# Optimization experiments

Measured on AMD Instinct MI355X. Metric: run time of the kernel, lower is better.

## Reference

```python
import jax, jax.numpy as jnp
import numpy as np

L = 2        # n_layers
F = 128      # in_features == out_features (GRUCell + highway constraint)
O = 128
N = 1024     # nodes
B = 8        # batch
D = 3        # edge directions (weight.size(0))


def setup_inputs() -> dict:
    key = jax.random.key(0)
    ks = jax.random.split(key, 10)
    s = 1.0 / np.sqrt(F)
    u = lambda k, shp: jax.random.uniform(k, shp, jnp.float32, minval=-s, maxval=s)
    return {
        "inputs": jax.random.normal(ks[0], (N, B, F), jnp.float32),
        "adj": jax.random.uniform(ks[1], (D, B, N, N), jnp.float32),
        "W": u(ks[2], (L, D, F, O)),            # GCN weight per layer/direction
        "Bc": u(ks[3], (L, D, O)),              # GCN bias
        "Wh": u(ks[4], (L, F, O)),              # highway weight
        "Bh": u(ks[5], (L, O)),                 # highway bias
        "Wih": u(ks[6], (L, 3 * O, O)),         # GRUCell input weights
        "Whh": u(ks[7], (L, 3 * O, O)),         # GRUCell hidden weights
        "bih": u(ks[8], (L, 3 * O)),
        "bhh": u(ks[9], (L, 3 * O)),
    }


def _gru(x, h, wih, whh, bih, bhh):
    # torch.nn.GRUCell semantics; x,h: [..., O]
    gi = x @ wih.T + bih
    gh = h @ whh.T + bhh
    i_r, i_z, i_n = jnp.split(gi, 3, axis=-1)
    h_r, h_z, h_n = jnp.split(gh, 3, axis=-1)
    r = jax.nn.sigmoid(i_r + h_r)
    z = jax.nn.sigmoid(i_z + h_z)
    n = jnp.tanh(i_n + r * h_n)
    return (1.0 - z) * n + z * h


def reference(inputs, adj, W, Bc, Wh, Bh, Wih, Whh, bih, bhh):
    x = inputs  # [N, B, F]; dropout layers are identity at eval
    for l in range(L):
        # support per direction: [D, B, N, O]
        support = jnp.einsum('nbf,dfo->dbno', x, W[l]) + Bc[l][:, None, None, :]
        # adjacency-weighted aggregation: adj[d,b] @ support[d,b]
        agg = jnp.einsum('dbmn,dbno->dbmo', adj, support)
        # GRU update with hidden = current features, per direction, summed over d
        h = jnp.broadcast_to(jnp.transpose(x, (1, 0, 2))[None], agg.shape)
        hnew = _gru(agg, h, Wih[l], Whh[l], bih[l], bhh[l])
        out = jnp.transpose(jnp.sum(hnew, axis=0), (1, 0, 2))  # [N, B, O]
        out = jax.nn.relu(out)  # activation='relu'
        # highway gate (highway='relu')
        t = jax.nn.relu(jnp.einsum('nbf,fo->nbo', x, Wh[l]) + Bh[l])
        x = out * t + x * (1.0 - t)
    return x
```

## Files before the change

kernel.cpp:

```cpp
#include <hip/hip_runtime.h>
#include <math.h>

#define N_NODES 1024
#define BATCH   8
#define FEAT    128
#define NDIR    3
#define NB      (N_NODES*BATCH)
#define G3      384

typedef __bf16 bf16_t;
using bf16x8 = __attribute__((ext_vector_type(8))) __bf16;
using bf16x4 = __attribute__((ext_vector_type(4))) __bf16;
using f32x4  = __attribute__((ext_vector_type(4))) float;

#define GLOAD_LDS16(g, l) \
    __builtin_amdgcn_global_load_lds((const __attribute__((address_space(1))) void*)(g), \
                                     (__attribute__((address_space(3))) void*)(l), 16, 0, 0)

template<int R>
__device__ __forceinline__ void stage_swz(const bf16_t* __restrict__ src, int stride,
                                          int k0, bf16_t* lds, int w, int lane)
{
    #pragma unroll
    for (int q = 0; q < R/32; ++q) {
        int rbase = w*(R/4) + q*8;
        int row = rbase + (lane >> 3);
        int seg = (lane & 7) ^ (row & 7);
        GLOAD_LDS16(src + (size_t)row*stride + k0 + seg*8,
                    (char*)lds + (size_t)rbase*128);
    }
}

__device__ __forceinline__ void stageA_f32(const float* __restrict__ src, int k0,
                                           bf16_t* lds, int w, int lane)
{
    #pragma unroll
    for (int q = 0; q < 2; ++q) {
        int rbase = w*16 + q*8;
        int row = rbase + (lane >> 3);
        int s   = lane & 7;
        int seg = s ^ (row & 7);
        const float* g = src + (size_t)row*1024 + k0 + seg*8;
        float4 v0 = *reinterpret_cast<const float4*>(g);
        float4 v1 = *reinterpret_cast<const float4*>(g + 4);
        bf16x8 pk;
        pk[0]=(bf16_t)(v0.x-0.5f); pk[1]=(bf16_t)(v0.y-0.5f);
        pk[2]=(bf16_t)(v0.z-0.5f); pk[3]=(bf16_t)(v0.w-0.5f);
        pk[4]=(bf16_t)(v1.x-0.5f); pk[5]=(bf16_t)(v1.y-0.5f);
        pk[6]=(bf16_t)(v1.z-0.5f); pk[7]=(bf16_t)(v1.w-0.5f);
        *reinterpret_cast<bf16x8*>(&lds[row*64 + s*8]) = pk;
    }
}

template<int MI, int NJ>
__device__ __forceinline__ void mfma_swz(const bf16_t* As, const bf16_t* Bs,
                                         f32x4 (&acc)[MI][NJ], int wr, int wc, int lane)
{
    #pragma unroll
    for (int ks = 0; ks < 64; ks += 32) {
        int bslot = ks/8 + (lane >> 4);
        int sx = bslot ^ (lane & 7);
        bf16x8 af[MI], bfv[NJ];
        #pragma unroll
        for (int i = 0; i < MI; ++i) {
            int row = wr*MI*16 + i*16 + (lane & 15);
            af[i] = *reinterpret_cast<const bf16x8*>(&As[row*64 + sx*8]);
        }
        #pragma unroll
        for (int j = 0; j < NJ; ++j) {
            int row = wc*NJ*16 + j*16 + (lane & 15);
            bfv[j] = *reinterpret_cast<const bf16x8*>(&Bs[row*64 + sx*8]);
        }
        #pragma unroll
        for (int i = 0; i < MI; ++i) {
            #pragma unroll
            for (int j = 0; j < NJ; ++j)
                acc[i][j] = __builtin_amdgcn_mfma_f32_16x16x32_bf16(af[i], bfv[j], acc[i][j], 0, 0, 0);
        }
    }
}

__device__ __forceinline__ float fast_sigmoid(float x)
{
    float t = __builtin_amdgcn_exp2f(-1.442695041f * x);
    return __builtin_amdgcn_rcpf(1.0f + t);
}
__device__ __forceinline__ float fast_tanh(float x)
{
    float ax = fabsf(x);
    float t = __builtin_amdgcn_exp2f(-2.885390082f * ax);
    float r = (1.0f - t) * __builtin_amdgcn_rcpf(1.0f + t);
    return copysignf(r, x);
}

__global__ __launch_bounds__(128) void k_wprep(
    const float* __restrict__ W, const float* __restrict__ Wh,
    const float* __restrict__ Whh, const float* __restrict__ Wih,
    bf16_t* __restrict__ wsup,
    bf16_t* __restrict__ wihc)
{
    int m = blockIdx.x, l = blockIdx.y, k = threadIdx.x;
    float w;
    bf16_t* dst;
    bool patB = false;
    if (m < 384) {
        int d = m >> 7, o = m & 127;
        w = W[((size_t)(l*3 + d)*128 + k)*128 + o];
        dst = wsup + ((size_t)l*896 + m)*384;
    } else if (m < 512) {
        int o = m - 384;
        w = Wh[((size_t)l*128 + k)*128 + o];
        dst = wsup + ((size_t)l*896 + m)*384;
    } else if (m < 896) {
        int c = m - 512;
        w = Whh[((size_t)l*384 + c)*128 + k];
        dst = wsup + ((size_t)l*896 + m)*384;
    } else {
        int c = m - 896;
        w = Wih[((size_t)l*384 + c)*128 + k];
        dst = wihc + ((size_t)l*384 + c)*384;
        patB = true;
    }
    bf16_t hi = (bf16_t)w;
    bf16_t lo = (bf16_t)(w - (float)hi);
    if (patB) { dst[k] = hi; dst[128 + k] = hi; dst[256 + k] = lo; }
    else      { dst[k] = hi; dst[128 + k] = lo; dst[256 + k] = hi; }
}

__global__ __launch_bounds__(256) void k_xcat(
    const float* __restrict__ X, bf16_t* __restrict__ xcat,
    float* __restrict__ colsum2)
{
    int idx = blockIdx.x * 256 + threadIdx.x;
    if (idx < 2*3072) colsum2[idx] = 0.0f;
    int k = idx & 127, r = idx >> 7;
    int n = r >> 3, b = r & 7;
    float v = X[idx];
    bf16_t hi = (bf16_t)v;
    bf16_t lo = (bf16_t)(v - (float)hi);
    bf16_t* dst = xcat + ((size_t)(b*1024 + n))*384 + k;
    dst[0] = hi; dst[128] = hi; dst[256] = lo;
}

__global__ __launch_bounds__(256, 2) void k_sup2(
    const bf16_t* __restrict__ Wcat,
    const bf16_t* __restrict__ xcat,
    const float* __restrict__ Bcl,
    const float* __restrict__ Bhl,
    const float* __restrict__ bhhl,
    bf16_t* __restrict__ supt,
    float* __restrict__ tbuf,
    bf16_t* __restrict__ ghb,
    float* __restrict__ colsum)
{
    __shared__ bf16_t As[2][128*64];
    __shared__ bf16_t Bs[2][128*64];
    const int t = threadIdx.x, lane = t & 63, w = t >> 6;
    const int wr = w >> 1, wc = w & 1;
    const int n0 = blockIdx.x * 128;
    const int m0 = blockIdx.y * 128;
    const int b  = blockIdx.z;
    const bf16_t* Arow = Wcat + (size_t)m0 * 384;
    const bf16_t* Brow = xcat + ((size_t)b * 1024 + n0) * 384;

    f32x4 acc[4][4] = {};
    stage_swz<128>(Arow, 384, 0, As[0], w, lane);
    stage_swz<128>(Brow, 384, 0, Bs[0], w, lane);
    __syncthreads();
    #pragma unroll
    for (int kt = 0; kt < 6; ++kt) {
        if (kt + 1 < 6) {
            stage_swz<128>(Arow, 384, (kt+1)*64, As[(kt+1)&1], w, lane);
            stage_swz<128>(Brow, 384, (kt+1)*64, Bs[(kt+1)&1], w, lane);
        }
        mfma_swz<4,4>(As[kt&1], Bs[kt&1], acc, wr, wc, lane);
        __syncthreads();
    }
    #pragma unroll
    for (int i = 0; i < 4; ++i) {
        int mb = m0 + wr*64 + i*16 + ((lane >> 4) * 4);
        if (mb < 384) {
            #pragma unroll
            for (int rg = 0; rg < 4; ++rg) {
                int m = mb + rg;
                int d = m >> 7, o = m & 127;
                float bv = Bcl[d*128 + o];
                float psum = 0.0f;
                #pragma unroll
                for (int j = 0; j < 4; ++j) {
                    int n = n0 + wc*64 + j*16 + (lane & 15);
                    bf16_t sv = (bf16_t)(acc[i][j][rg] + bv);
                    supt[((size_t)((d*8 + b)*128 + o))*1024 + n] = sv;
                    psum += (float)sv;
                }
                psum += __shfl_xor(psum, 1, 64);
                psum += __shfl_xor(psum, 2, 64);
                psum += __shfl_xor(psum, 4, 64);
                psum += __shfl_xor(psum, 8, 64);
                if ((lane & 15) == 0)
                    atomicAdd(&colsum[(d*8 + b)*128 + o], psum);
            }
        } else if (mb < 512) {
            #pragma unroll
            for (int j = 0; j < 4; ++j) {
                int n = n0 + wc*64 + j*16 + (lane & 15);
                #pragma unroll
                for (int rg = 0; rg < 4; ++rg) {
                    int o = mb + rg - 384;
                    tbuf[((size_t)(b*128 + o))*1024 + n] =
                        fmaxf(acc[i][j][rg] + Bhl[o], 0.0f);
                }
            }
        } else {
            #pragma unroll
            for (int j = 0; j < 4; ++j) {
                int n = n0 + wc*64 + j*16 + (lane & 15);
                int c = mb - 512;
                bf16x4 pk;
                #pragma unroll
                for (int rg = 0; rg < 4; ++rg)
                    pk[rg] = (bf16_t)(acc[i][j][rg] + bhhl[c + rg]);
                *reinterpret_cast<bf16x4*>(&ghb[((size_t)(b*1024 + n))*384 + c]) = pk;
            }
        }
    }
}

__device__ __forceinline__ int aggls_off(int row, int k)
{
    return row*256 + (((k >> 3) ^ (row & 15)) << 3) + (k & 7);
}

__global__ __launch_bounds__(256, 2) void k_aggi(
    const float* __restrict__ adjf,
    const bf16_t* __restrict__ supt,
    const float* __restrict__ colsum,
    const bf16_t* __restrict__ wihcL,
    const float* __restrict__ biasL,
    bf16_t* __restrict__ girz,
    float* __restrict__ gin)
{
    __shared__ char pool[49152];
    __shared__ bf16_t aggls[64*256];
    bf16_t* As  = (bf16_t*)pool;
    bf16_t* Bs  = (bf16_t*)(pool + 16384);
    bf16_t* BsG = (bf16_t*)pool;

    const int t = threadIdx.x, lane = t & 63, w = t >> 6;
    const int wr = w >> 1, wc = w & 1;
    const int m0 = blockIdx.x * 64;
    const int z  = blockIdx.y;
    const float*  Af   = adjf + (size_t)z * 1024 * 1024 + (size_t)m0 * 1024;
    const bf16_t* Brow = supt + (size_t)z * 128 * 1024;

    f32x4 acc[2][4] = {};
    stageA_f32(Af, 0, As, w, lane);
    stage_swz<128>(Brow, 1024, 0, Bs, w, lane);
    __syncthreads();
    #pragma unroll
    for (int kt = 0; kt < 16; ++kt) {
        if (kt + 1 < 16) {
            stageA_f32(Af, (kt+1)*64, As + ((kt+1)&1)*4096, w, lane);
            stage_swz<128>(Brow, 1024, (kt+1)*64, Bs + ((kt+1)&1)*8192, w, lane);
        }
        mfma_swz<2,4>(As + (kt&1)*4096, Bs + (kt&1)*8192, acc, wr, wc, lane);
        __syncthreads();
    }

    stage_swz<128>(wihcL, 384, 0, BsG, w, lane);

    #pragma unroll
    for (int i = 0; i < 2; ++i) {
        #pragma unroll
        for (int rg = 0; rg < 4; ++rg) {
            int row = wr*32 + i*16 + ((lane >> 4) * 4) + rg;
            #pragma unroll
            for (int j = 0; j < 4; ++j) {
                int o = wc*64 + j*16 + (lane & 15);
                float v = acc[i][j][rg] + 0.5f * colsum[z*128 + o];
                bf16_t hi = (bf16_t)v;
                bf16_t lo = (bf16_t)(v - (float)hi);
                aggls[aggls_off(row, o)]       = hi;
                aggls[aggls_off(row, 128 + o)] = lo;
            }
        }
    }
    __syncthreads();

    #pragma unroll
    for (int cc = 0; cc < 3; ++cc) {
        f32x4 a2[2][4] = {};
        #pragma unroll
        for (int kt = 0; kt < 6; ++kt) {
            int it = cc*6 + kt;
            if (it + 1 < 18) {
                int nc = (it+1)/6, nk = (it+1)%6;
                stage_swz<128>(wihcL + (size_t)nc*128*384, 384, nk*64,
                               BsG + ((it+1)&1)*8192, w, lane);
            }
            const bf16_t* Bcur = BsG + (it&1)*8192;
            int akk = (kt < 4 ? kt : kt - 4) * 64;
            #pragma unroll
            for (int ks = 0; ks < 64; ks += 32) {
                bf16x8 af[2], bfv[4];
                #pragma unroll
                for (int i = 0; i < 2; ++i) {
                    int row = wr*32 + i*16 + (lane & 15);
                    int ss = ((akk + ks)/8 + (lane >> 4)) ^ (lane & 15);
                    af[i] = *reinterpret_cast<const bf16x8*>(&aggls[row*256 + ss*8]);
                }
                #pragma unroll
                for (int j = 0; j < 4; ++j) {
                    int row = wc*64 + j*16 + (lane & 15);
                    int sx = (ks/8 + (lane >> 4)) ^ (lane & 7);
                    bfv[j] = *reinterpret_cast<const bf16x8*>(&Bcur[row*64 + sx*8]);
                }
                #pragma unroll
                for (int i = 0; i < 2; ++i) {
                    #pragma unroll
                    for (int j = 0; j < 4; ++j)
                        a2[i][j] = __builtin_amdgcn_mfma_f32_16x16x32_bf16(af[i], bfv[j], a2[i][j], 0, 0, 0);
                }
            }
            __syncthreads();
        }
        #pragma unroll
        for (int j = 0; j < 4; ++j) {
            int c = cc*128 + wc*64 + j*16 + (lane & 15);
            float bv = biasL[c];
            #pragma unroll
            for (int i = 0; i < 2; ++i) {
                #pragma unroll
                for (int rg = 0; rg < 4; ++rg) {
                    int rloc = wr*32 + i*16 + ((lane >> 4) * 4) + rg;
                    size_t m = (size_t)z*1024 + m0 + rloc;
                    float v = a2[i][j][rg] + bv;
                    if (c < 256) girz[m*256 + c] = (bf16_t)v;
                    else         gin[m*128 + (c - 256)] = v;
                }
            }
        }
    }
}

__global__ __launch_bounds__(256) void k_gates(
    const bf16_t* __restrict__ girz, const float* __restrict__ gin,
    const bf16_t* __restrict__ ghb,
    bf16_t* xcat,
    const float* __restrict__ tbuf,
    float* __restrict__ Xout, int write_xcat)
{
    __shared__ float ts[128*17];
    const int b = blockIdx.y, n0 = blockIdx.x * 16;
    const int tid = threadIdx.x;
    {
        int o = tid >> 1, nh = (tid & 1) * 8;
        const float* src = tbuf + ((size_t)(b*128 + o))*1024 + n0 + nh;
        float4 v0 = *reinterpret_cast<const float4*>(src);
        float4 v1 = *reinterpret_cast<const float4*>(src + 4);
        float* dst = &ts[o*17 + nh];
        dst[0]=v0.x; dst[1]=v0.y; dst[2]=v0.z; dst[3]=v0.w;
        dst[4]=v1.x; dst[5]=v1.y; dst[6]=v1.z; dst[7]=v1.w;
    }
    __syncthreads();
    #pragma unroll
    for (int p = 0; p < 8; ++p) {
        int e = p*256 + tid;
        int nn = e >> 7, o = e & 127;
        int n = n0 + nn;
        size_t rb = (size_t)(b*1024 + n);
        bf16_t* xr = xcat + rb*384;
        float h = (float)xr[o] + (float)xr[256 + o];
        const bf16_t* ghr = ghb + rb*G3;
        float g_r = (float)ghr[o], g_z = (float)ghr[128+o], g_n = (float)ghr[256+o];
        float acc = 0.0f;
        #pragma unroll
        for (int d = 0; d < 3; ++d) {
            size_t rr = (size_t)((d*8 + b)*1024 + n);
            float i_r = (float)girz[rr*256 + o];
            float i_z = (float)girz[rr*256 + 128 + o];
            float i_n = gin[rr*128 + o];
            float rg = fast_sigmoid(i_r + g_r);
            float zg = fast_sigmoid(i_z + g_z);
            float ng = fast_tanh(i_n + rg * g_n);
            acc += (1.0f - zg) * ng + zg * h;
        }
        float outv = fmaxf(acc, 0.0f);
        float tg = ts[o*17 + nn];
        float res = outv * tg + h * (1.0f - tg);
        if (Xout) Xout[(size_t)(n*8 + b)*128 + o] = res;
        if (write_xcat) {
            bf16_t hi = (bf16_t)res;
            bf16_t lo = (bf16_t)(res - (float)hi);
            xr[o] = hi; xr[128 + o] = hi; xr[256 + o] = lo;
        }
    }
}

extern "C" void kernel_launch(void* const* d_in, const int* in_sizes, int n_in,
                              void* d_out, int out_size, void* d_ws, size_t ws_size,
                              hipStream_t stream) {
    const float* inputs = (const float*)d_in[0];
    const float* adj    = (const float*)d_in[1];
    const float* W      = (const float*)d_in[2];
    const float* Bc     = (const float*)d_in[3];
    const float* Wh     = (const float*)d_in[4];
    const float* Bh     = (const float*)d_in[5];
    const float* Wih    = (const float*)d_in[6];
    const float* Whh    = (const float*)d_in[7];
    const float* bih    = (const float*)d_in[8];
    const float* bhh    = (const float*)d_in[9];

    char* ws = (char*)d_ws;
    float*  tbuf   = (float*)ws;   ws += (size_t)8*128*1024*4;
    bf16_t* xcat   = (bf16_t*)ws;  ws += (size_t)8*1024*384*2;
    bf16_t* ghb    = (bf16_t*)ws;  ws += (size_t)NB*G3*2;
    bf16_t* supt   = (bf16_t*)ws;  ws += (size_t)24*128*1024*2;
    bf16_t* girz   = (bf16_t*)ws;  ws += (size_t)3*NB*256*2;
    float*  gin    = (float*)ws;   ws += (size_t)3*NB*128*4;
    float*  colsum2= (float*)ws;   ws += (size_t)2*24*128*4;
    bf16_t* wsup   = (bf16_t*)ws;  ws += (size_t)2*896*384*2;
    bf16_t* wihc   = (bf16_t*)ws;

    k_wprep<<<dim3(1280, 2), dim3(128), 0, stream>>>(W, Wh, Whh, Wih, wsup, wihc);
    k_xcat<<<dim3(4096), dim3(256), 0, stream>>>(inputs, xcat, colsum2);

    for (int l = 0; l < 2; ++l) {
        float* colsum = colsum2 + l*3072;
        k_sup2<<<dim3(8, 7, 8), dim3(256), 0, stream>>>(
            wsup + (size_t)l*896*384, xcat, Bc + l*3*128, Bh + l*128, bhh + l*G3,
            supt, tbuf, ghb, colsum);
        k_aggi<<<dim3(16, 24), dim3(256), 0, stream>>>(
            adj, supt, colsum, wihc + (size_t)l*384*384, bih + l*G3, girz, gin);
        k_gates<<<dim3(64, 8), dim3(256), 0, stream>>>(
            girz, gin, ghb, xcat, tbuf,
            (l == 1) ? (float*)d_out : (float*)nullptr, (l == 0) ? 1 : 0);
    }
}
```

Before: 294.5 us.

## Pre-convert adjacency to bf16 once and triple-buffer k_aggi with async LDS loads

Adds a kernel that converts the fp32 adjacency, shifted by 0.5, to bf16 once up front, so both layers read half the bytes and can use direct global-to-LDS loads instead of register staging. k_aggi moves to 32-row tiles (twice the blocks) with a 3-stage ring buffer, explicit vmcnt waits, raw barriers and setprio around the MFMAs. The GRU input GEMM is pipelined the same way. The extra conversion pass reads the full fp32 adjacency once and writes a bf16 copy, and the smaller tiles reload support rows more often.

```diff
diff --git a/kernel.cpp b/kernel.cpp
--- a/kernel.cpp
+++ b/kernel.cpp
@@ -17,6 +17,10 @@
     __builtin_amdgcn_global_load_lds((const __attribute__((address_space(1))) void*)(g), \
                                      (__attribute__((address_space(3))) void*)(l), 16, 0, 0)
 
+#define WAITV(N) asm volatile("s_waitcnt vmcnt(" #N ")" ::: "memory")
+#define BARRIER_PL asm volatile("s_barrier" ::: "memory")
+#define BARRIER_LG asm volatile("s_waitcnt lgkmcnt(0)\n\ts_barrier" ::: "memory")
+
 template<int R>
 __device__ __forceinline__ void stage_swz(const bf16_t* __restrict__ src, int stride,
                                           int k0, bf16_t* lds, int w, int lane)
@@ -31,27 +35,6 @@
     }
 }
 
-__device__ __forceinline__ void stageA_f32(const float* __restrict__ src, int k0,
-                                           bf16_t* lds, int w, int lane)
-{
-    #pragma unroll
-    for (int q = 0; q < 2; ++q) {
-        int rbase = w*16 + q*8;
-        int row = rbase + (lane >> 3);
-        int s   = lane & 7;
-        int seg = s ^ (row & 7);
-        const float* g = src + (size_t)row*1024 + k0 + seg*8;
-        float4 v0 = *reinterpret_cast<const float4*>(g);
-        float4 v1 = *reinterpret_cast<const float4*>(g + 4);
-        bf16x8 pk;
-        pk[0]=(bf16_t)(v0.x-0.5f); pk[1]=(bf16_t)(v0.y-0.5f);
-        pk[2]=(bf16_t)(v0.z-0.5f); pk[3]=(bf16_t)(v0.w-0.5f);
-        pk[4]=(bf16_t)(v1.x-0.5f); pk[5]=(bf16_t)(v1.y-0.5f);
-        pk[6]=(bf16_t)(v1.z-0.5f); pk[7]=(bf16_t)(v1.w-0.5f);
-        *reinterpret_cast<bf16x8*>(&lds[row*64 + s*8]) = pk;
-    }
-}
-
 template<int MI, int NJ>
 __device__ __forceinline__ void mfma_swz(const bf16_t* As, const bf16_t* Bs,
                                          f32x4 (&acc)[MI][NJ], int wr, int wc, int lane)
@@ -91,6 +74,20 @@
     float t = __builtin_amdgcn_exp2f(-2.885390082f * ax);
     float r = (1.0f - t) * __builtin_amdgcn_rcpf(1.0f + t);
     return copysignf(r, x);
+}
+
+__global__ __launch_bounds__(256) void k_cvt_adj(
+    const float* __restrict__ src, bf16_t* __restrict__ dst, int n4)
+{
+    int i = blockIdx.x * 256 + threadIdx.x;
+    int stride = gridDim.x * 256;
+    for (; i < n4; i += stride) {
+        float4 v = reinterpret_cast<const float4*>(src)[i];
+        bf16x4 o;
+        o[0] = (bf16_t)(v.x - 0.5f); o[1] = (bf16_t)(v.y - 0.5f);
+        o[2] = (bf16_t)(v.z - 0.5f); o[3] = (bf16_t)(v.w - 0.5f);
+        *reinterpret_cast<bf16x4*>(&dst[(size_t)i * 4]) = o;
+    }
 }
 
 __global__ __launch_bounds__(128) void k_wprep(
@@ -232,7 +229,7 @@
 }
 
 __global__ __launch_bounds__(256, 2) void k_aggi(
-    const float* __restrict__ adjf,
+    const bf16_t* __restrict__ adjb,
     const bf16_t* __restrict__ supt,
     const float* __restrict__ colsum,
     const bf16_t* __restrict__ wihcL,
@@ -240,74 +237,83 @@
     bf16_t* __restrict__ girz,
     float* __restrict__ gin)
 {
-    __shared__ char pool[49152];
-    __shared__ bf16_t aggls[64*256];
-    bf16_t* As  = (bf16_t*)pool;
-    bf16_t* Bs  = (bf16_t*)(pool + 16384);
-    bf16_t* BsG = (bf16_t*)pool;
+    __shared__ char pool[61440];
+    __shared__ bf16_t aggls[32*256];
+    bf16_t* AsP = (bf16_t*)pool;
+    bf16_t* BsP = (bf16_t*)(pool + 12288);
+    bf16_t* BgP = (bf16_t*)pool;
 
     const int t = threadIdx.x, lane = t & 63, w = t >> 6;
     const int wr = w >> 1, wc = w & 1;
-    const int m0 = blockIdx.x * 64;
+    const int m0 = blockIdx.x * 32;
     const int z  = blockIdx.y;
-    const float*  Af   = adjf + (size_t)z * 1024 * 1024 + (size_t)m0 * 1024;
-    const bf16_t* Brow = supt + (size_t)z * 128 * 1024;
-
-    f32x4 acc[2][4] = {};
-    stageA_f32(Af, 0, As, w, lane);
-    stage_swz<128>(Brow, 1024, 0, Bs, w, lane);
-    __syncthreads();
+    const bf16_t* Arow = adjb + (size_t)z*1024*1024 + (size_t)m0*1024;
+    const bf16_t* Brow = supt + (size_t)z*128*1024;
+
+    float cs[4];
+    #pragma unroll
+    for (int j = 0; j < 4; ++j)
+        cs[j] = colsum[z*128 + wc*64 + j*16 + (lane & 15)];
+
+    stage_swz<32>(Arow, 1024, 0, AsP, w, lane);
+    stage_swz<128>(Brow, 1024, 0, BsP, w, lane);
+    stage_swz<32>(Arow, 1024, 64, AsP + 2048, w, lane);
+    stage_swz<128>(Brow, 1024, 64, BsP + 8192, w, lane);
+    stage_swz<32>(Arow, 1024, 128, AsP + 4096, w, lane);
+    stage_swz<128>(Brow, 1024, 128, BsP + 16384, w, lane);
+    WAITV(10);
+    BARRIER_PL;
+
+    f32x4 acc[1][4] = {};
     #pragma unroll
     for (int kt = 0; kt < 16; ++kt) {
-        if (kt + 1 < 16) {
-            stageA_f32(Af, (kt+1)*64, As + ((kt+1)&1)*4096, w, lane);
-            stage_swz<128>(Brow, 1024, (kt+1)*64, Bs + ((kt+1)&1)*8192, w, lane);
-        }
-        mfma_swz<2,4>(As + (kt&1)*4096, Bs + (kt&1)*8192, acc, wr, wc, lane);
-        __syncthreads();
-    }
-
-    stage_swz<128>(wihcL, 384, 0, BsG, w, lane);
-
-    #pragma unroll
-    for (int i = 0; i < 2; ++i) {
+        __builtin_amdgcn_s_setprio(1);
+        mfma_swz<1,4>(AsP + (kt%3)*2048, BsP + (kt%3)*8192, acc, wr, wc, lane);
+        __builtin_amdgcn_s_setprio(0);
+        if (kt <= 13)      { WAITV(5); }
+        else if (kt == 14) { WAITV(0); }
+        BARRIER_PL;
+        if (kt + 3 < 16) {
+            stage_swz<128>(Brow, 1024, (kt+3)*64, BsP + ((kt+3)%3)*8192, w, lane);
+            stage_swz<32>(Arow, 1024, (kt+3)*64, AsP + ((kt+3)%3)*2048, w, lane);
+        }
+    }
+
+    stage_swz<128>(wihcL, 384, 0, BgP, w, lane);
+    #pragma unroll
+    for (int j = 0; j < 4; ++j) {
+        int o = wc*64 + j*16 + (lane & 15);
         #pragma unroll
         for (int rg = 0; rg < 4; ++rg) {
-            int row = wr*32 + i*16 + ((lane >> 4) * 4) + rg;
-            #pragma unroll
-            for (int j = 0; j < 4; ++j) {
-                int o = wc*64 + j*16 + (lane & 15);
-                float v = acc[i][j][rg] + 0.5f * colsum[z*128 + o];
-                bf16_t hi = (bf16_t)v;
-                bf16_t lo = (bf16_t)(v - (float)hi);
-                aggls[aggls_off(row, o)]       = hi;
-                aggls[aggls_off(row, 128 + o)] = lo;
-            }
-        }
-    }
-    __syncthreads();
-
+            int row = wr*16 + ((lane >> 4) * 4) + rg;
+            float v = acc[0][j][rg] + 0.5f * cs[j];
+            bf16_t hi = (bf16_t)v;
+            bf16_t lo = (bf16_t)(v - (float)hi);
+            aggls[aggls_off(row, o)]       = hi;
+            aggls[aggls_off(row, 128 + o)] = lo;
+        }
+    }
+    stage_swz<128>(wihcL, 384, 64,  BgP + 8192,  w, lane);
+    stage_swz<128>(wihcL, 384, 128, BgP + 16384, w, lane);
+    WAITV(8);
+    BARRIER_LG;
+
+    f32x4 a2[3][4] = {};
     #pragma unroll
     for (int cc = 0; cc < 3; ++cc) {
-        f32x4 a2[2][4] = {};
-        #pragma unroll
-        for (int kt = 0; kt < 6; ++kt) {
-            int it = cc*6 + kt;
-            if (it + 1 < 18) {
-                int nc = (it+1)/6, nk = (it+1)%6;
-                stage_swz<128>(wihcL + (size_t)nc*128*384, 384, nk*64,
-                               BsG + ((it+1)&1)*8192, w, lane);
-            }
-            const bf16_t* Bcur = BsG + (it&1)*8192;
-            int akk = (kt < 4 ? kt : kt - 4) * 64;
+        #pragma unroll
+        for (int kt6 = 0; kt6 < 6; ++kt6) {
+            const int it = cc*6 + kt6;
+            const bf16_t* Bcur = BgP + (it%3)*8192;
+            int akk = (kt6 < 4 ? kt6 : kt6 - 4) * 64;
+            __builtin_amdgcn_s_setprio(1);
             #pragma unroll
             for (int ks = 0; ks < 64; ks += 32) {
-                bf16x8 af[2], bfv[4];
-                #pragma unroll
-                for (int i = 0; i < 2; ++i) {
-                    int row = wr*32 + i*16 + (lane & 15);
+                bf16x8 af, bfv[4];
+                {
+                    int row = wr*16 + (lane & 15);
                     int ss = ((akk + ks)/8 + (lane >> 4)) ^ (lane & 15);
-                    af[i] = *reinterpret_cast<const bf16x8*>(&aggls[row*256 + ss*8]);
+                    af = *reinterpret_cast<const bf16x8*>(&aggls[row*256 + ss*8]);
                 }
                 #pragma unroll
                 for (int j = 0; j < 4; ++j) {
@@ -316,28 +322,34 @@
                     bfv[j] = *reinterpret_cast<const bf16x8*>(&Bcur[row*64 + sx*8]);
                 }
                 #pragma unroll
-                for (int i = 0; i < 2; ++i) {
-                    #pragma unroll
-                    for (int j = 0; j < 4; ++j)
-                        a2[i][j] = __builtin_amdgcn_mfma_f32_16x16x32_bf16(af[i], bfv[j], a2[i][j], 0, 0, 0);
-                }
-            }
-            __syncthreads();
-        }
+                for (int j = 0; j < 4; ++j)
+                    a2[cc][j] = __builtin_amdgcn_mfma_f32_16x16x32_bf16(af, bfv[j], a2[cc][j], 0, 0, 0);
+            }
+            __builtin_amdgcn_s_setprio(0);
+            if (it <= 15)      { WAITV(4); }
+            else if (it == 16) { WAITV(0); }
+            BARRIER_PL;
+            if (it + 3 < 18) {
+                const int ni = it + 3;
+                stage_swz<128>(wihcL + (size_t)(ni/6)*128*384, 384, (ni%6)*64,
+                               BgP + (ni%3)*8192, w, lane);
+            }
+        }
+    }
+
+    #pragma unroll
+    for (int cc = 0; cc < 3; ++cc) {
         #pragma unroll
         for (int j = 0; j < 4; ++j) {
             int c = cc*128 + wc*64 + j*16 + (lane & 15);
             float bv = biasL[c];
             #pragma unroll
-            for (int i = 0; i < 2; ++i) {
-                #pragma unroll
-                for (int rg = 0; rg < 4; ++rg) {
-                    int rloc = wr*32 + i*16 + ((lane >> 4) * 4) + rg;
-                    size_t m = (size_t)z*1024 + m0 + rloc;
-                    float v = a2[i][j][rg] + bv;
-                    if (c < 256) girz[m*256 + c] = (bf16_t)v;
-                    else         gin[m*128 + (c - 256)] = v;
-                }
+            for (int rg = 0; rg < 4; ++rg) {
+                int rloc = wr*16 + ((lane >> 4) * 4) + rg;
+                size_t m = (size_t)z*1024 + m0 + rloc;
+                float v = a2[cc][j][rg] + bv;
+                if (c < 256) girz[m*256 + c] = (bf16_t)v;
+                else         gin[m*128 + (c - 256)] = v;
             }
         }
     }
@@ -420,8 +432,10 @@
     float*  gin    = (float*)ws;   ws += (size_t)3*NB*128*4;
     float*  colsum2= (float*)ws;   ws += (size_t)2*24*128*4;
     bf16_t* wsup   = (bf16_t*)ws;  ws += (size_t)2*896*384*2;
-    bf16_t* wihc   = (bf16_t*)ws;
-
+    bf16_t* wihc   = (bf16_t*)ws;  ws += (size_t)2*384*384*2;
+    bf16_t* adjb   = (bf16_t*)ws;
+
+    k_cvt_adj<<<dim3(4096), dim3(256), 0, stream>>>(adj, adjb, 3*8*1024*1024/4);
     k_wprep<<<dim3(1280, 2), dim3(128), 0, stream>>>(W, Wh, Whh, Wih, wsup, wihc);
     k_xcat<<<dim3(4096), dim3(256), 0, stream>>>(inputs, xcat, colsum2);
 
@@ -430,8 +444,8 @@
         k_sup2<<<dim3(8, 7, 8), dim3(256), 0, stream>>>(
             wsup + (size_t)l*896*384, xcat, Bc + l*3*128, Bh + l*128, bhh + l*G3,
             supt, tbuf, ghb, colsum);
-        k_aggi<<<dim3(16, 24), dim3(256), 0, stream>>>(
-            adj, supt, colsum, wihc + (size_t)l*384*384, bih + l*G3, girz, gin);
+        k_aggi<<<dim3(32, 24), dim3(256), 0, stream>>>(
+            adjb, supt, colsum, wihc + (size_t)l*384*384, bih + l*G3, girz, gin);
         k_gates<<<dim3(64, 8), dim3(256), 0, stream>>>(
             girz, gin, ghb, xcat, tbuf,
             (l == 1) ? (float*)d_out : (float*)nullptr, (l == 0) ? 1 : 0);
```

Result: slower. 312.6 us (+6.2%).
